# Performance work log

Measured on AMD Instinct MI355X. Metric: run time of the kernel, lower is better.

## Reference

```python
import jax, jax.numpy as jnp
import numpy as np
from functools import partial

DIM = 1024
LIGHT_HID = 512   # dim * 0.5
HEAVY_HID = 4096  # dim * 4
NUM_HEAVY = 1024
N_ITERS = 50
K_ROUTE = 8.0
EPS = 0.1


def rms_norm(x, gamma):
    # F.normalize(x, dim=-1) * sqrt(dim) * gamma
    norm = jnp.linalg.norm(x, axis=-1, keepdims=True)
    normed = x / jnp.maximum(norm, 1e-12)
    return normed * (x.shape[-1] ** 0.5) * gamma


def ffn(x, gamma, w1, b1, w2, b2):
    h = rms_norm(x, gamma)
    h = jax.nn.gelu(h @ w1 + b1, approximate=False)
    return h @ w2 + b2


def coor_descent_route(x, routing_token, num_tokens):
    # s: [b, n]
    s = jnp.einsum('bnd,d->bn', x, routing_token)
    constant = EPS * jnp.log(jnp.asarray(K_ROUTE, dtype=s.dtype))
    b0 = -jax.nn.relu(s)
    a0 = jnp.zeros((s.shape[0], 1), dtype=s.dtype)

    def step(carry, _):
        a_prev, b = carry
        a = constant - EPS * jax.nn.logsumexp((s + b) / EPS, axis=-1, keepdims=True)
        b = -jax.nn.relu(s + a)
        return (a, b), None

    (a, b), _ = jax.lax.scan(step, (a0, b0), None, length=N_ITERS)
    scores = jnp.exp((s + a + b) / EPS)
    sel_scores, sel_idx = jax.lax.top_k(scores, num_tokens)
    # straight-through: value -> 1.0, gradient -> d(sel_scores)
    sel_scores = sel_scores + jax.lax.stop_gradient(1.0 - sel_scores)
    return sel_scores, sel_idx


def setup_inputs() -> dict:
    key = jax.random.key(0)
    ks = jax.random.split(key, 12)
    def lin(k, fan_in, fan_out):
        lim = 1.0 / np.sqrt(fan_in)
        kw, kb = jax.random.split(k)
        w = jax.random.uniform(kw, (fan_in, fan_out), jnp.float32, -lim, lim)
        b = jax.random.uniform(kb, (fan_out,), jnp.float32, -lim, lim)
        return w, b
    x = jax.random.normal(ks[0], (4, 8192, DIM), jnp.float32)
    routing_token = jax.random.normal(ks[1], (DIM,), jnp.float32)
    gamma_light = jnp.ones((DIM,), jnp.float32)
    w1_l, b1_l = lin(ks[2], DIM, LIGHT_HID)
    w2_l, b2_l = lin(ks[3], LIGHT_HID, DIM)
    gamma_heavy = jnp.ones((DIM,), jnp.float32)
    w1_h, b1_h = lin(ks[4], DIM, HEAVY_HID)
    w2_h, b2_h = lin(ks[5], HEAVY_HID, DIM)
    return dict(x=x, routing_token=routing_token,
                gamma_light=gamma_light, w1_light=w1_l, b1_light=b1_l,
                w2_light=w2_l, b2_light=b2_l,
                gamma_heavy=gamma_heavy, w1_heavy=w1_h, b1_heavy=b1_h,
                w2_heavy=w2_h, b2_heavy=b2_h)


def reference(x, routing_token, gamma_light, w1_light, b1_light, w2_light, b2_light,
              gamma_heavy, w1_heavy, b1_heavy, w2_heavy, b2_heavy):
    bsz = x.shape[0]
    light_out = ffn(x, gamma_light, w1_light, b1_light, w2_light, b2_light)
    sel_scores, sel_idx = coor_descent_route(x, routing_token, NUM_HEAVY)
    batch_range = jnp.arange(bsz)[:, None]           # [b, 1]
    routed = x[batch_range, sel_idx]                 # [b, k, d]
    routed_out = ffn(routed, gamma_heavy, w1_heavy, b1_heavy, w2_heavy, b2_heavy)
    routed_out = routed_out * sel_scores[..., None]
    heavy_out = jnp.zeros_like(x).at[batch_range, sel_idx].set(routed_out)
    return light_out + heavy_out
```

## Files before the change

kernel.cpp:

```cpp
#include <hip/hip_runtime.h>
#include <math.h>

#define TOKS   32768
#define NSEQ   8192
#define BATCH  4
#define DIMD   1024
#define LHID   512
#define HHID   4096
#define NHEAVY 1024

typedef __attribute__((ext_vector_type(8))) short bf16x8;
typedef __attribute__((ext_vector_type(4))) float f32x4;
typedef __attribute__((ext_vector_type(8))) unsigned short u16x8;
typedef __attribute__((ext_vector_type(4))) unsigned short u16x4;

__device__ __forceinline__ unsigned short bf16rne(float f) {
    unsigned u = __float_as_uint(f);
    return (unsigned short)((u + 0x7FFFu + ((u >> 16) & 1u)) >> 16);
}
__device__ __forceinline__ float gelu_f(float v) {
    return 0.5f * v * (1.0f + erff(v * 0.7071067811865476f));
}
__device__ __forceinline__ void gload_lds16(const unsigned short* g, unsigned short* l) {
#if defined(__HIP_DEVICE_COMPILE__)
    __builtin_amdgcn_global_load_lds((const __attribute__((address_space(1))) void*)g,
                                     (__attribute__((address_space(3))) void*)l,
                                     16, 0, 0);
#endif
}

__global__ __launch_bounds__(256) void k_rowscale(const float* __restrict__ x,
                                                  const float* __restrict__ rt,
                                                  const float* __restrict__ gamma,
                                                  float* __restrict__ s,
                                                  float* __restrict__ invr,
                                                  unsigned short* __restrict__ xl) {
    int wid = threadIdx.x >> 6, lane = threadIdx.x & 63;
    int row = blockIdx.x * 4 + wid;
    const float4* xr  = (const float4*)(x + (size_t)row * DIMD);
    const float4* rt4 = (const float4*)rt;
    const float4* g4  = (const float4*)gamma;
    float4 v[4];
    float dot = 0.f, ss = 0.f;
#pragma unroll
    for (int i = 0; i < 4; i++) {
        v[i] = xr[lane + 64 * i];
        float4 r = rt4[lane + 64 * i];
        dot += v[i].x * r.x + v[i].y * r.y + v[i].z * r.z + v[i].w * r.w;
        ss  += v[i].x * v[i].x + v[i].y * v[i].y + v[i].z * v[i].z + v[i].w * v[i].w;
    }
#pragma unroll
    for (int o = 32; o > 0; o >>= 1) {
        dot += __shfl_xor(dot, o);
        ss  += __shfl_xor(ss, o);
    }
    float iv = 32.0f / fmaxf(sqrtf(ss), 1e-12f);
    if (lane == 0) { s[row] = dot; invr[row] = iv; }
#pragma unroll
    for (int i = 0; i < 4; i++) {
        float4 g = g4[lane + 64 * i];
        u16x4 o;
        o[0] = bf16rne(v[i].x * iv * g.x);
        o[1] = bf16rne(v[i].y * iv * g.y);
        o[2] = bf16rne(v[i].z * iv * g.z);
        o[3] = bf16rne(v[i].w * iv * g.w);
        *(u16x4*)(xl + (size_t)row * DIMD + (lane + 64 * i) * 4) = o;
    }
}

__global__ __launch_bounds__(256) void k_rowstats(const float* __restrict__ x,
                                                  const float* __restrict__ rt,
                                                  float* __restrict__ s,
                                                  float* __restrict__ invr) {
    int wid = threadIdx.x >> 6, lane = threadIdx.x & 63;
    int row = blockIdx.x * 4 + wid;
    const float4* xr  = (const float4*)(x + (size_t)row * DIMD);
    const float4* rt4 = (const float4*)rt;
    float dot = 0.f, ss = 0.f;
#pragma unroll
    for (int i = 0; i < 4; i++) {
        float4 v = xr[lane + 64 * i];
        float4 r = rt4[lane + 64 * i];
        dot += v.x * r.x + v.y * r.y + v.z * r.z + v.w * r.w;
        ss  += v.x * v.x + v.y * v.y + v.z * v.z + v.w * v.w;
    }
#pragma unroll
    for (int o = 32; o > 0; o >>= 1) {
        dot += __shfl_down(dot, o);
        ss  += __shfl_down(ss, o);
    }
    if (lane == 0) {
        s[row] = dot;
        invr[row] = 32.0f / fmaxf(sqrtf(ss), 1e-12f);
    }
}

__global__ __launch_bounds__(1024) void k_route(const float* __restrict__ s_g,
                                                unsigned long long* __restrict__ keys,
                                                int* __restrict__ pcount,
                                                int* __restrict__ c1cnt) {
    int b = blockIdx.x, tid = threadIdx.x;
    int lane = tid & 63, wid = tid >> 6;
    const float* sb = s_g + b * NSEQ;
    float sv[8];
    float smax = -3.4e38f;
#pragma unroll
    for (int i = 0; i < 8; i++) { sv[i] = sb[tid + 1024 * i]; smax = fmaxf(smax, sv[i]); }
    __shared__ float red[2][16];
#pragma unroll
    for (int o = 32; o > 0; o >>= 1) smax = fmaxf(smax, __shfl_xor(smax, o));
    if (lane == 0) red[0][wid] = smax;
    __syncthreads();
    float smaxAll = -3.4e38f;
    for (int w = 0; w < 16; w++) smaxAll = fmaxf(smaxAll, red[0][w]);
    __syncthreads();

    const float cst = 0.1f * logf(8.0f);
    float a = 0.0f;
    for (int it = 0; it < 50; it++) {
        float tau = -a;
        float M = fminf(smaxAll, tau);
        float p = 0.0f;
#pragma unroll
        for (int i = 0; i < 8; i++) p += expf((fminf(sv[i], tau) - M) * 10.0f);
#pragma unroll
        for (int o = 32; o > 0; o >>= 1) p += __shfl_xor(p, o);
        if (lane == 0) red[it & 1][wid] = p;
        __syncthreads();
        float S = 0.0f;
        for (int w = 0; w < 16; w++) S += red[it & 1][w];
        a = cst - M - 0.1f * logf(S);
    }
    int p = 0, c1 = 0;
#pragma unroll
    for (int i = 0; i < 8; i++) {
        float sc = expf(fminf(sv[i] + a, 0.0f) * 10.0f);
        int n = tid + 1024 * i;
        keys[b * NSEQ + n] = ((unsigned long long)__float_as_uint(sc) << 32)
                           | (unsigned long long)(0xFFFFFFFFu - (unsigned)n);
        p  += (sc > 0.0f) ? 1 : 0;
        c1 += (sc == 1.0f) ? 1 : 0;
    }
#pragma unroll
    for (int o = 32; o > 0; o >>= 1) {
        p  += __shfl_xor(p, o);
        c1 += __shfl_xor(c1, o);
    }
    if (lane == 0) { atomicAdd(&pcount[b], p); atomicAdd(&c1cnt[b], c1); }
}

__global__ __launch_bounds__(1024) void k_select(const unsigned long long* __restrict__ keys,
                                                 const int* __restrict__ pcount,
                                                 const int* __restrict__ c1cnt,
                                                 int* __restrict__ rowmap) {
    int b = blockIdx.x, tid = threadIdx.x;
    int lane = tid & 63, wid = tid >> 6;
    __shared__ int wsum[16];
    __shared__ int slot;
    __shared__ unsigned long long kk_[NSEQ];
    int P = pcount[b], C1 = c1cnt[b];
    if (C1 >= NHEAVY) {
        bool f[8]; int zc = 0;
#pragma unroll
        for (int j = 0; j < 8; j++) {
            unsigned hi = (unsigned)(keys[b * NSEQ + tid * 8 + j] >> 32);
            f[j] = (hi == 0x3F800000u);
            zc += f[j] ? 1 : 0;
        }
        int inc = zc;
        for (int o = 1; o < 64; o <<= 1) {
            int t = __shfl_up(inc, o);
            if (lane >= o) inc += t;
        }
        if (lane == 63) wsum[wid] = inc;
        __syncthreads();
        if (tid == 0) {
            int acc = 0;
            for (int w = 0; w < 16; w++) { int t = wsum[w]; wsum[w] = acc; acc += t; }
        }
        __syncthreads();
        int rank = wsum[wid] + (inc - zc);
#pragma unroll
        for (int j = 0; j < 8; j++) {
            if (f[j]) {
                if (rank < NHEAVY) rowmap[b * NHEAVY + rank] = b * NSEQ + tid * 8 + j;
                rank++;
            }
        }
    } else if (P <= NHEAVY) {
        bool pos[8]; int zc = 0;
#pragma unroll
        for (int j = 0; j < 8; j++) {
            unsigned sbits = (unsigned)(keys[b * NSEQ + tid * 8 + j] >> 32);
            pos[j] = (sbits != 0u);
            zc += pos[j] ? 0 : 1;
        }
        int inc = zc;
        for (int o = 1; o < 64; o <<= 1) {
            int t = __shfl_up(inc, o);
            if (lane >= o) inc += t;
        }
        if (lane == 63) wsum[wid] = inc;
        if (tid == 0) slot = 0;
        __syncthreads();
        if (tid == 0) {
            int acc = 0;
            for (int w = 0; w < 16; w++) { int t = wsum[w]; wsum[w] = acc; acc += t; }
        }
        __syncthreads();
        int zr = wsum[wid] + (inc - zc);
        int Z = NHEAVY - P;
#pragma unroll
        for (int j = 0; j < 8; j++) {
            int n = tid * 8 + j;
            bool sel;
            if (pos[j]) sel = true;
            else { sel = (zr < Z); zr += 1; }
            if (sel) {
                int sl = atomicAdd(&slot, 1);
                rowmap[b * NHEAVY + sl] = b * NSEQ + n;
            }
        }
    } else {
        for (int i = tid; i < NSEQ; i += 1024) kk_[i] = keys[b * NSEQ + i];
        __syncthreads();
        for (int k = 2; k <= NSEQ; k <<= 1) {
            for (int j = k >> 1; j > 0; j >>= 1) {
                for (int i = tid; i < NSEQ; i += 1024) {
                    int ixj = i ^ j;
                    if (ixj > i) {
                        unsigned long long u = kk_[i], v = kk_[ixj];
                        bool dirDesc = ((i & k) == 0);
                        if (dirDesc ? (u < v) : (u > v)) { kk_[i] = v; kk_[ixj] = u; }
                    }
                }
                __syncthreads();
            }
        }
        unsigned idx = 0xFFFFFFFFu - (unsigned)(kk_[tid] & 0xFFFFFFFFull);
        rowmap[b * NHEAVY + tid] = b * NSEQ + (int)idx;
    }
}

__global__ __launch_bounds__(256) void k_transpose(const float* __restrict__ W,
                                                   unsigned short* __restrict__ WT,
                                                   int K, int N) {
    __shared__ float ts[64][65];
    int t = threadIdx.x;
    int n0 = blockIdx.x * 64, k0 = blockIdx.y * 64;
    int kk = t >> 2, nc = (t & 3) * 16;
    const float4* src = (const float4*)(W + (size_t)(k0 + kk) * N + n0 + nc);
#pragma unroll
    for (int j = 0; j < 4; j++) {
        float4 v = src[j];
        ts[kk][nc + 4 * j + 0] = v.x;
        ts[kk][nc + 4 * j + 1] = v.y;
        ts[kk][nc + 4 * j + 2] = v.z;
        ts[kk][nc + 4 * j + 3] = v.w;
    }
    __syncthreads();
    int nn = t >> 2, kc = (t & 3) * 16;
    unsigned short o[16];
#pragma unroll
    for (int j = 0; j < 16; j++) o[j] = bf16rne(ts[kc + j][nn]);
    unsigned short* dst = WT + (size_t)(n0 + nn) * K + k0 + kc;
    *(u16x8*)(dst)     = *(u16x8*)(o);
    *(u16x8*)(dst + 8) = *(u16x8*)(o + 8);
}

__global__ __launch_bounds__(256) void k_prescale(const float* __restrict__ x,
                                                  const float* __restrict__ invr,
                                                  const float* __restrict__ gamma,
                                                  const int* __restrict__ rowmap,
                                                  unsigned short* __restrict__ xo,
                                                  int row_ofs) {
    int t = threadIdx.x;
    int i = blockIdx.x * 2 + (t >> 7);
    int c = (t & 127) * 8;
    int src = rowmap ? rowmap[i] : (row_ofs + i);
    float iv = invr[src];
    const float4* px = (const float4*)(x + (size_t)src * DIMD + c);
    const float4* pg = (const float4*)(gamma + c);
    float4 v0 = px[0], v1 = px[1];
    float4 g0 = pg[0], g1 = pg[1];
    unsigned short o[8];
    o[0] = bf16rne(v0.x * iv * g0.x); o[1] = bf16rne(v0.y * iv * g0.y);
    o[2] = bf16rne(v0.z * iv * g0.z); o[3] = bf16rne(v0.w * iv * g0.w);
    o[4] = bf16rne(v1.x * iv * g1.x); o[5] = bf16rne(v1.y * iv * g1.y);
    o[6] = bf16rne(v1.z * iv * g1.z); o[7] = bf16rne(v1.w * iv * g1.w);
    *(u16x8*)(xo + (size_t)i * DIMD + c) = *(u16x8*)o;
}

__global__ __launch_bounds__(256) void k_scatter(const float* __restrict__ rb,
                                                 const int* __restrict__ rowmap,
                                                 float* __restrict__ out) {
    int i = blockIdx.x;
    int c = threadIdx.x * 4;
    int g = rowmap[i];
    float4 v = *(const float4*)(rb + (size_t)i * DIMD + c);
    float* p = out + (size_t)g * DIMD + c;
    float4 o = *(const float4*)p;
    o.x += v.x; o.y += v.y; o.z += v.z; o.w += v.w;
    *(float4*)p = o;
}

struct GArg {
    const unsigned short* A; const unsigned short* BT; const float* bias;
    void* C; const int* rowmap;
    int K, kslice, m_ofs, ldc, nx, ny;
};

template<int EPI>
__device__ __forceinline__ void gemm_body(const GArg ga, int w, int nwg,
                                          unsigned short* As, unsigned short* Bs) {
    int tid = threadIdx.x;
    int q = nwg >> 3, r = nwg & 7;
    int xcd = w & 7, sub = w >> 3;
    int id = (xcd < r ? xcd * (q + 1) : r * (q + 1) + (xcd - r) * q) + sub;
    int bx = id % ga.nx;
    int t2 = id / ga.nx;
    int by = t2 % ga.ny;
    int bz = t2 / ga.ny;

    int m0 = by * 128, n0 = bx * 128;
    int kbeg = bz * ga.kslice, kend = kbeg + ga.kslice;
    int K = ga.K;
    int lane = tid & 63, wid = tid >> 6;
    int wm = wid >> 1, wn = wid & 1;
    int lc = lane & 15, lr = lane >> 4;

    int srow = lane >> 3;
    int sslot = (lane & 7) ^ srow;
    const unsigned short* paA = ga.A  + (size_t)(m0 + srow) * K + sslot * 8;
    const unsigned short* paB = ga.BT + (size_t)(n0 + srow) * K + sslot * 8;

    f32x4 acc[4][4];
#pragma unroll
    for (int i = 0; i < 4; i++)
#pragma unroll
        for (int j = 0; j < 4; j++) acc[i][j] = (f32x4){0.f, 0.f, 0.f, 0.f};

    for (int k0 = kbeg; k0 < kend; k0 += 64) {
        if (k0 != kbeg) __syncthreads();
#pragma unroll
        for (int qq = 0; qq < 4; qq++) {
            int rb_ = (wid * 4 + qq) * 8;
            gload_lds16(paA + (size_t)rb_ * K + k0, &As[rb_ * 64]);
            gload_lds16(paB + (size_t)rb_ * K + k0, &Bs[rb_ * 64]);
        }
        __syncthreads();
#pragma unroll
        for (int ks = 0; ks < 2; ks++) {
            bf16x8 af[4], bfr[4];
#pragma unroll
            for (int f = 0; f < 4; f++) {
                int rowA = wm * 64 + f * 16 + lc;
                int rowB = wn * 64 + f * 16 + lc;
                int sw = ((ks * 4 + lr) ^ (lc & 7)) << 4;
                af[f]  = *(const bf16x8*)((const char*)As + rowA * 128 + sw);
                bfr[f] = *(const bf16x8*)((const char*)Bs + rowB * 128 + sw);
            }
#pragma unroll
            for (int fm = 0; fm < 4; fm++)
#pragma unroll
                for (int fn = 0; fn < 4; fn++)
                    acc[fm][fn] = __builtin_amdgcn_mfma_f32_16x16x32_bf16(
                        af[fm], bfr[fn], acc[fm][fn], 0, 0, 0);
        }
    }

    float bcol[4];
#pragma unroll
    for (int fn = 0; fn < 4; fn++) {
        float bb = ga.bias[n0 + wn * 64 + fn * 16 + lc];
        if constexpr (EPI == 3) { if (bz != 0) bb = 0.0f; }
        bcol[fn] = bb;
    }
#pragma unroll
    for (int fm = 0; fm < 4; fm++) {
        int rowb = m0 + wm * 64 + fm * 16 + lr * 4;
#pragma unroll
        for (int fn = 0; fn < 4; fn++) {
            int col = n0 + wn * 64 + fn * 16 + lc;
            f32x4 v = acc[fm][fn];
#pragma unroll
            for (int rr = 0; rr < 4; rr++) {
                float val = v[rr] + bcol[fn];
                if constexpr (EPI == 0) {
                    ((unsigned short*)ga.C)[(size_t)(rowb + rr) * ga.ldc + col] =
                        bf16rne(gelu_f(val));
                } else if constexpr (EPI == 1) {
                    ((float*)ga.C)[(size_t)(ga.m_ofs + rowb + rr) * ga.ldc + col] = val;
                } else if constexpr (EPI == 2) {
                    int g = ga.rowmap[ga.m_ofs + rowb + rr];
                    float* p = (float*)ga.C + (size_t)g * ga.ldc + col;
                    *p = *p + val;
                } else {
                    int g = ga.rowmap ? ga.rowmap[rowb + rr] : (rowb + rr);
                    atomicAdd((float*)ga.C + (size_t)g * ga.ldc + col, val);
                }
            }
        }
    }
}

template<int EPI>
__global__ __launch_bounds__(256, 4) void k_mfma(GArg ga) {
    __shared__ unsigned short sm[2][128 * 64];
    gemm_body<EPI>(ga, (int)blockIdx.x, (int)gridDim.x, sm[0], sm[1]);
}

template<int EA, int EB>
__global__ __launch_bounds__(256, 4) void k_mfma2(GArg a, GArg b, int nwgA) {
    __shared__ unsigned short sm[2][128 * 64];
    int w = (int)blockIdx.x;
    if (w < nwgA) gemm_body<EA>(a, w, nwgA, sm[0], sm[1]);
    else          gemm_body<EB>(b, w - nwgA, (int)gridDim.x - nwgA, sm[0], sm[1]);
}

extern "C" void kernel_launch(void* const* d_in, const int* in_sizes, int n_in,
                              void* d_out, int out_size, void* d_ws, size_t ws_size,
                              hipStream_t stream) {
    const float* x   = (const float*)d_in[0];
    const float* rt  = (const float*)d_in[1];
    const float* gl  = (const float*)d_in[2];
    const float* w1l = (const float*)d_in[3];
    const float* b1l = (const float*)d_in[4];
    const float* w2l = (const float*)d_in[5];
    const float* b2l = (const float*)d_in[6];
    const float* gh  = (const float*)d_in[7];
    const float* w1h = (const float*)d_in[8];
    const float* b1h = (const float*)d_in[9];
    const float* w2h = (const float*)d_in[10];
    const float* b2h = (const float*)d_in[11];
    float* out = (float*)d_out;

    char* ws = (char*)d_ws;
    float* s    = (float*)(ws);
    float* invr = (float*)(ws + 131072);
    unsigned long long* keys = (unsigned long long*)(ws + 262144);
    int* rowmap = (int*)(ws + 524288);
    int* pcount = (int*)(ws + 540672);
    int* c1cnt  = pcount + 4;
    size_t off = 1u << 20;
    unsigned short* w1lT = (unsigned short*)(ws + off); off += (size_t)LHID * DIMD * 2;
    unsigned short* w2lT = (unsigned short*)(ws + off); off += (size_t)DIMD * LHID * 2;
    unsigned short* w1hT = (unsigned short*)(ws + off); off += (size_t)HHID * DIMD * 2;
    unsigned short* w2hT = (unsigned short*)(ws + off); off += (size_t)DIMD * HHID * 2;
    unsigned short* xhg  = (unsigned short*)(ws + off); off += (size_t)BATCH * NHEAVY * DIMD * 2;
    char* un = ws + off;
    size_t U = ws_size > off ? ws_size - off : 0;

    const size_t XL_B = (size_t)TOKS * DIMD * 2;
    const size_t HL_B = (size_t)TOKS * LHID * 2;
    const size_t HH_B = (size_t)BATCH * NHEAVY * HHID * 2;
    bool big = (U >= XL_B + HL_B + HH_B);

    hipMemsetAsync(pcount, 0, 32, stream);

    const long MH = (long)BATCH * NHEAVY;

    if (big) {
        unsigned short* xl = (unsigned short*)un;
        unsigned short* hl = (unsigned short*)(un + XL_B);
        unsigned short* hh = (unsigned short*)(un + XL_B + HL_B);
        float* rb = (float*)un;

        k_rowscale<<<TOKS / 4, 256, 0, stream>>>(x, rt, gl, s, invr, xl);
        k_route<<<BATCH, 1024, 0, stream>>>(s, keys, pcount, c1cnt);
        k_select<<<BATCH, 1024, 0, stream>>>(keys, pcount, c1cnt, rowmap);

        k_transpose<<<dim3(LHID / 64, DIMD / 64), 256, 0, stream>>>(w1l, w1lT, DIMD, LHID);
        k_transpose<<<dim3(DIMD / 64, LHID / 64), 256, 0, stream>>>(w2l, w2lT, LHID, DIMD);
        k_transpose<<<dim3(HHID / 64, DIMD / 64), 256, 0, stream>>>(w1h, w1hT, DIMD, HHID);
        k_transpose<<<dim3(DIMD / 64, HHID / 64), 256, 0, stream>>>(w2h, w2hT, HHID, DIMD);
        k_prescale<<<(unsigned)(MH / 2), 256, 0, stream>>>(x, invr, gh, rowmap, xhg, 0);

        GArg lg1{xl,  w1lT, b1l, hl, nullptr, DIMD, DIMD, 0, LHID, LHID / 128, TOKS / 128};
        GArg hg1{xhg, w1hT, b1h, hh, nullptr, DIMD, DIMD, 0, HHID, HHID / 128, (int)MH / 128};
        k_mfma2<0, 0><<<2048, 256, 0, stream>>>(lg1, hg1, 1024);

        hipMemsetAsync(rb, 0, (size_t)MH * DIMD * 4, stream);
        GArg lg2{hl, w2lT, b2l, out, nullptr, LHID, LHID, 0, DIMD, DIMD / 128, TOKS / 128};
        GArg hg2{hh, w2hT, b2h, rb, nullptr, HHID, HHID / 4, 0, DIMD, DIMD / 128, (int)MH / 128};
        k_mfma2<1, 3><<<3072, 256, 0, stream>>>(lg2, hg2, 2048);

        k_scatter<<<(unsigned)MH, 256, 0, stream>>>(rb, rowmap, out);
    } else {
        k_rowstats<<<TOKS / 4, 256, 0, stream>>>(x, rt, s, invr);
        k_route<<<BATCH, 1024, 0, stream>>>(s, keys, pcount, c1cnt);
        k_select<<<BATCH, 1024, 0, stream>>>(keys, pcount, c1cnt, rowmap);

        k_transpose<<<dim3(LHID / 64, DIMD / 64), 256, 0, stream>>>(w1l, w1lT, DIMD, LHID);
        k_transpose<<<dim3(DIMD / 64, LHID / 64), 256, 0, stream>>>(w2l, w2lT, LHID, DIMD);
        k_transpose<<<dim3(HHID / 64, DIMD / 64), 256, 0, stream>>>(w1h, w1hT, DIMD, HHID);
        k_transpose<<<dim3(DIMD / 64, HHID / 64), 256, 0, stream>>>(w2h, w2hT, HHID, DIMD);

        long Rl = (long)(U / 3072);
        Rl -= Rl % 128; if (Rl < 128) Rl = 128; if (Rl > TOKS) Rl = TOKS;
        unsigned short* xl = (unsigned short*)un;
        unsigned short* hl = (unsigned short*)(un + (size_t)Rl * DIMD * 2);
        for (long mo = 0; mo < TOKS; mo += Rl) {
            long R = TOKS - mo < Rl ? TOKS - mo : Rl;
            k_prescale<<<(unsigned)(R / 2), 256, 0, stream>>>(x, invr, gl, nullptr, xl, (int)mo);
            GArg a1{xl, w1lT, b1l, hl, nullptr, DIMD, DIMD, 0, LHID, LHID / 128, (int)(R / 128)};
            k_mfma<0><<<(LHID / 128) * (unsigned)(R / 128), 256, 0, stream>>>(a1);
            GArg a2{hl, w2lT, b2l, out, nullptr, LHID, LHID, (int)mo, DIMD, DIMD / 128, (int)(R / 128)};
            k_mfma<1><<<(DIMD / 128) * (unsigned)(R / 128), 256, 0, stream>>>(a2);
        }

        k_prescale<<<(unsigned)(MH / 2), 256, 0, stream>>>(x, invr, gh, rowmap, xhg, 0);
        long Rh = (long)(U / ((size_t)HHID * 2));
        Rh -= Rh % 128; if (Rh < 128) Rh = 128; if (Rh > MH) Rh = MH;
        unsigned short* hh = (unsigned short*)un;
        for (long mo = 0; mo < MH; mo += Rh) {
            long R = MH - mo < Rh ? MH - mo : Rh;
            GArg b1{xhg + (size_t)mo * DIMD, w1hT, b1h, hh, nullptr, DIMD, DIMD, 0, HHID,
                    HHID / 128, (int)(R / 128)};
            k_mfma<0><<<(HHID / 128) * (unsigned)(R / 128), 256, 0, stream>>>(b1);
            GArg b2{hh, w2hT, b2h, out, rowmap, HHID, HHID, (int)mo, DIMD,
                    DIMD / 128, (int)(R / 128)};
            k_mfma<2><<<(DIMD / 128) * (unsigned)(R / 128), 256, 0, stream>>>(b2);
        }
    }
}
```

Before: 392.8 us.

## Fuse routing and selection, batch transposes, drop split-K and reorder GEMM work

Merges the route and select kernels into one per-batch kernel that builds the row map directly, with fast paths that skip the bitonic sort. It also combines the four weight transposes into one launch and removes the pcount and accumulator memsets. The heavy second GEMM no longer uses split-K with an atomic epilogue, and heavy work-groups are scheduled ahead of light ones. The GEMM loop now uses pointer increments and the occupancy hint goes from 4 to 5. These changes cut launch overhead and atomic traffic, but without split-K the heavy GEMM has fewer, longer work-groups, which can leave the tail of the grid unbalanced.

```diff
diff --git a/kernel.cpp b/kernel.cpp
--- a/kernel.cpp
+++ b/kernel.cpp
@@ -95,6 +95,164 @@
     }
 }
 
+__global__ __launch_bounds__(1024) void k_routesel(const float* __restrict__ s_g,
+                                                   int* __restrict__ rowmap) {
+    int b = blockIdx.x, tid = threadIdx.x;
+    int lane = tid & 63, wid = tid >> 6;
+    __shared__ float red[2][16];
+    __shared__ int wsum[16];
+    __shared__ int ws2[16];
+    __shared__ int PC[2];
+    __shared__ int slot;
+    __shared__ unsigned long long kk_[NSEQ];
+    const float* sb = s_g + b * NSEQ;
+    float sv[8];
+    float smax = -3.4e38f;
+#pragma unroll
+    for (int i = 0; i < 8; i++) { sv[i] = sb[tid + 1024 * i]; smax = fmaxf(smax, sv[i]); }
+#pragma unroll
+    for (int o = 32; o > 0; o >>= 1) smax = fmaxf(smax, __shfl_xor(smax, o));
+    if (lane == 0) red[0][wid] = smax;
+    __syncthreads();
+    float smaxAll = -3.4e38f;
+    for (int w = 0; w < 16; w++) smaxAll = fmaxf(smaxAll, red[0][w]);
+    __syncthreads();
+
+    const float cst = 0.1f * logf(8.0f);
+    float a = 0.0f;
+    for (int it = 0; it < 50; it++) {
+        float tau = -a;
+        float M = fminf(smaxAll, tau);
+        float p = 0.0f;
+#pragma unroll
+        for (int i = 0; i < 8; i++) p += expf((fminf(sv[i], tau) - M) * 10.0f);
+#pragma unroll
+        for (int o = 32; o > 0; o >>= 1) p += __shfl_xor(p, o);
+        if (lane == 0) red[it & 1][wid] = p;
+        __syncthreads();
+        float S = 0.0f;
+        for (int w = 0; w < 16; w++) S += red[it & 1][w];
+        a = cst - M - 0.1f * logf(S);
+        __syncthreads();
+    }
+    float sc[8];
+    int p = 0, c1 = 0;
+#pragma unroll
+    for (int i = 0; i < 8; i++) {
+        sc[i] = expf(fminf(sv[i] + a, 0.0f) * 10.0f);
+        p  += (sc[i] > 0.0f) ? 1 : 0;
+        c1 += (sc[i] == 1.0f) ? 1 : 0;
+    }
+    {
+        int pp = p, cc = c1;
+#pragma unroll
+        for (int o = 32; o > 0; o >>= 1) {
+            pp += __shfl_xor(pp, o);
+            cc += __shfl_xor(cc, o);
+        }
+        if (lane == 0) { wsum[wid] = pp; ws2[wid] = cc; }
+        __syncthreads();
+        if (tid == 0) {
+            int sp = 0, sC = 0;
+            for (int w = 0; w < 16; w++) { sp += wsum[w]; sC += ws2[w]; }
+            PC[0] = sp; PC[1] = sC;
+        }
+        __syncthreads();
+    }
+    int P = PC[0], C1 = PC[1];
+    __syncthreads();
+
+    if (C1 >= NHEAVY) {
+        __shared__ unsigned char fl[NSEQ];
+#pragma unroll
+        for (int i = 0; i < 8; i++) fl[tid + 1024 * i] = (sc[i] == 1.0f) ? 1 : 0;
+        __syncthreads();
+        int zc = 0;
+        unsigned char f[8];
+#pragma unroll
+        for (int j = 0; j < 8; j++) { f[j] = fl[tid * 8 + j]; zc += f[j]; }
+        int inc = zc;
+        for (int o = 1; o < 64; o <<= 1) {
+            int t = __shfl_up(inc, o);
+            if (lane >= o) inc += t;
+        }
+        if (lane == 63) wsum[wid] = inc;
+        __syncthreads();
+        if (tid == 0) {
+            int acc = 0;
+            for (int w = 0; w < 16; w++) { int t = wsum[w]; wsum[w] = acc; acc += t; }
+        }
+        __syncthreads();
+        int rank = wsum[wid] + (inc - zc);
+#pragma unroll
+        for (int j = 0; j < 8; j++) {
+            if (f[j]) {
+                if (rank < NHEAVY) rowmap[b * NHEAVY + rank] = b * NSEQ + tid * 8 + j;
+                rank++;
+            }
+        }
+    } else if (P <= NHEAVY) {
+        __shared__ unsigned char fl[NSEQ];
+#pragma unroll
+        for (int i = 0; i < 8; i++) fl[tid + 1024 * i] = (sc[i] > 0.0f) ? 1 : 0;
+        __syncthreads();
+        unsigned char pos[8]; int zc = 0;
+#pragma unroll
+        for (int j = 0; j < 8; j++) { pos[j] = fl[tid * 8 + j]; zc += pos[j] ? 0 : 1; }
+        int inc = zc;
+        for (int o = 1; o < 64; o <<= 1) {
+            int t = __shfl_up(inc, o);
+            if (lane >= o) inc += t;
+        }
+        if (lane == 63) wsum[wid] = inc;
+        if (tid == 0) slot = 0;
+        __syncthreads();
+        if (tid == 0) {
+            int acc = 0;
+            for (int w = 0; w < 16; w++) { int t = wsum[w]; wsum[w] = acc; acc += t; }
+        }
+        __syncthreads();
+        int zr = wsum[wid] + (inc - zc);
+        int Z = NHEAVY - P;
+#pragma unroll
+        for (int j = 0; j < 8; j++) {
+            int n = tid * 8 + j;
+            bool sel;
+            if (pos[j]) sel = true;
+            else { sel = (zr < Z); zr += 1; }
+            if (sel) {
+                int sl = atomicAdd(&slot, 1);
+                rowmap[b * NHEAVY + sl] = b * NSEQ + n;
+            }
+        }
+    } else {
+#pragma unroll
+        for (int i = 0; i < 8; i++) {
+            int n = tid + 1024 * i;
+            kk_[n] = ((unsigned long long)__float_as_uint(sc[i]) << 32)
+                   | (unsigned long long)(0xFFFFFFFFu - (unsigned)n);
+        }
+        __syncthreads();
+        for (int k = 2; k <= NSEQ; k <<= 1) {
+            for (int j = k >> 1; j > 0; j >>= 1) {
+                for (int i = tid; i < NSEQ; i += 1024) {
+                    int ixj = i ^ j;
+                    if (ixj > i) {
+                        unsigned long long u = kk_[i], v = kk_[ixj];
+                        bool dirDesc = ((i & k) == 0);
+                        if (dirDesc ? (u < v) : (u > v)) { kk_[i] = v; kk_[ixj] = u; }
+                    }
+                }
+                __syncthreads();
+            }
+        }
+        if (tid < NHEAVY) {
+            unsigned idx = 0xFFFFFFFFu - (unsigned)(kk_[tid] & 0xFFFFFFFFull);
+            rowmap[b * NHEAVY + tid] = b * NSEQ + (int)idx;
+        }
+    }
+}
+
 __global__ __launch_bounds__(1024) void k_route(const float* __restrict__ s_g,
                                                 unsigned long long* __restrict__ keys,
                                                 int* __restrict__ pcount,
@@ -114,7 +272,6 @@
     float smaxAll = -3.4e38f;
     for (int w = 0; w < 16; w++) smaxAll = fmaxf(smaxAll, red[0][w]);
     __syncthreads();
-
     const float cst = 0.1f * logf(8.0f);
     float a = 0.0f;
     for (int it = 0; it < 50; it++) {
@@ -242,12 +399,10 @@
     }
 }
 
-__global__ __launch_bounds__(256) void k_transpose(const float* __restrict__ W,
-                                                   unsigned short* __restrict__ WT,
-                                                   int K, int N) {
+__device__ __forceinline__ void transpose_body(const float* W, unsigned short* WT,
+                                               int K, int N, int n0, int k0) {
     __shared__ float ts[64][65];
     int t = threadIdx.x;
-    int n0 = blockIdx.x * 64, k0 = blockIdx.y * 64;
     int kk = t >> 2, nc = (t & 3) * 16;
     const float4* src = (const float4*)(W + (size_t)(k0 + kk) * N + n0 + nc);
 #pragma unroll
@@ -266,6 +421,24 @@
     unsigned short* dst = WT + (size_t)(n0 + nn) * K + k0 + kc;
     *(u16x8*)(dst)     = *(u16x8*)(o);
     *(u16x8*)(dst + 8) = *(u16x8*)(o + 8);
+}
+
+__global__ __launch_bounds__(256) void k_transpose(const float* __restrict__ W,
+                                                   unsigned short* __restrict__ WT,
+                                                   int K, int N) {
+    transpose_body(W, WT, K, N, blockIdx.x * 64, blockIdx.y * 64);
+}
+
+__global__ __launch_bounds__(256) void k_transpose4(
+        const float* w1l, unsigned short* w1lT,
+        const float* w2l, unsigned short* w2lT,
+        const float* w1h, unsigned short* w1hT,
+        const float* w2h, unsigned short* w2hT) {
+    int w = (int)blockIdx.x;
+    if (w < 128)       { int i = w;        transpose_body(w1l, w1lT, DIMD, LHID, (i % 8) * 64,  (i / 8) * 64); }
+    else if (w < 256)  { int i = w - 128;  transpose_body(w2l, w2lT, LHID, DIMD, (i % 16) * 64, (i / 16) * 64); }
+    else if (w < 1280) { int i = w - 256;  transpose_body(w1h, w1hT, DIMD, HHID, (i % 64) * 64, (i / 64) * 64); }
+    else               { int i = w - 1280; transpose_body(w2h, w2hT, HHID, DIMD, (i % 16) * 64, (i / 16) * 64); }
 }
 
 __global__ __launch_bounds__(256) void k_prescale(const float* __restrict__ x,
@@ -323,7 +496,8 @@
     int bz = t2 / ga.ny;
 
     int m0 = by * 128, n0 = bx * 128;
-    int kbeg = bz * ga.kslice, kend = kbeg + ga.kslice;
+    int kbeg = bz * ga.kslice;
+    int nsteps = ga.kslice >> 6;
     int K = ga.K;
     int lane = tid & 63, wid = tid >> 6;
     int wm = wid >> 1, wn = wid & 1;
@@ -331,8 +505,21 @@
 
     int srow = lane >> 3;
     int sslot = (lane & 7) ^ srow;
-    const unsigned short* paA = ga.A  + (size_t)(m0 + srow) * K + sslot * 8;
-    const unsigned short* paB = ga.BT + (size_t)(n0 + srow) * K + sslot * 8;
+    const unsigned short* paA = ga.A  + (size_t)(m0 + srow) * K + sslot * 8 + kbeg;
+    const unsigned short* paB = ga.BT + (size_t)(n0 + srow) * K + sslot * 8 + kbeg;
+
+    const unsigned short* gA[4];
+    const unsigned short* gB[4];
+    unsigned short* lA[4];
+    unsigned short* lB[4];
+#pragma unroll
+    for (int qq = 0; qq < 4; qq++) {
+        int rb_ = (wid * 4 + qq) * 8;
+        gA[qq] = paA + (size_t)rb_ * K;
+        gB[qq] = paB + (size_t)rb_ * K;
+        lA[qq] = &As[rb_ * 64];
+        lB[qq] = &Bs[rb_ * 64];
+    }
 
     f32x4 acc[4][4];
 #pragma unroll
@@ -340,13 +527,13 @@
 #pragma unroll
         for (int j = 0; j < 4; j++) acc[i][j] = (f32x4){0.f, 0.f, 0.f, 0.f};
 
-    for (int k0 = kbeg; k0 < kend; k0 += 64) {
-        if (k0 != kbeg) __syncthreads();
+    for (int t = 0; t < nsteps; t++) {
+        if (t) __syncthreads();
 #pragma unroll
         for (int qq = 0; qq < 4; qq++) {
-            int rb_ = (wid * 4 + qq) * 8;
-            gload_lds16(paA + (size_t)rb_ * K + k0, &As[rb_ * 64]);
-            gload_lds16(paB + (size_t)rb_ * K + k0, &Bs[rb_ * 64]);
+            gload_lds16(gA[qq], lA[qq]);
+            gload_lds16(gB[qq], lB[qq]);
+            gA[qq] += 64; gB[qq] += 64;
         }
         __syncthreads();
 #pragma unroll
@@ -405,13 +592,13 @@
 }
 
 template<int EPI>
-__global__ __launch_bounds__(256, 4) void k_mfma(GArg ga) {
+__global__ __launch_bounds__(256, 5) void k_mfma(GArg ga) {
     __shared__ unsigned short sm[2][128 * 64];
     gemm_body<EPI>(ga, (int)blockIdx.x, (int)gridDim.x, sm[0], sm[1]);
 }
 
 template<int EA, int EB>
-__global__ __launch_bounds__(256, 4) void k_mfma2(GArg a, GArg b, int nwgA) {
+__global__ __launch_bounds__(256, 5) void k_mfma2(GArg a, GArg b, int nwgA) {
     __shared__ unsigned short sm[2][128 * 64];
     int w = (int)blockIdx.x;
     if (w < nwgA) gemm_body<EA>(a, w, nwgA, sm[0], sm[1]);
@@ -456,8 +643,6 @@
     const size_t HH_B = (size_t)BATCH * NHEAVY * HHID * 2;
     bool big = (U >= XL_B + HL_B + HH_B);
 
-    hipMemsetAsync(pcount, 0, 32, stream);
-
     const long MH = (long)BATCH * NHEAVY;
 
     if (big) {
@@ -467,26 +652,21 @@
         float* rb = (float*)un;
 
         k_rowscale<<<TOKS / 4, 256, 0, stream>>>(x, rt, gl, s, invr, xl);
-        k_route<<<BATCH, 1024, 0, stream>>>(s, keys, pcount, c1cnt);
-        k_select<<<BATCH, 1024, 0, stream>>>(keys, pcount, c1cnt, rowmap);
-
-        k_transpose<<<dim3(LHID / 64, DIMD / 64), 256, 0, stream>>>(w1l, w1lT, DIMD, LHID);
-        k_transpose<<<dim3(DIMD / 64, LHID / 64), 256, 0, stream>>>(w2l, w2lT, LHID, DIMD);
-        k_transpose<<<dim3(HHID / 64, DIMD / 64), 256, 0, stream>>>(w1h, w1hT, DIMD, HHID);
-        k_transpose<<<dim3(DIMD / 64, HHID / 64), 256, 0, stream>>>(w2h, w2hT, HHID, DIMD);
+        k_routesel<<<BATCH, 1024, 0, stream>>>(s, rowmap);
+        k_transpose4<<<2304, 256, 0, stream>>>(w1l, w1lT, w2l, w2lT, w1h, w1hT, w2h, w2hT);
         k_prescale<<<(unsigned)(MH / 2), 256, 0, stream>>>(x, invr, gh, rowmap, xhg, 0);
 
+        GArg hg1{xhg, w1hT, b1h, hh, nullptr, DIMD, DIMD, 0, HHID, HHID / 128, (int)MH / 128};
         GArg lg1{xl,  w1lT, b1l, hl, nullptr, DIMD, DIMD, 0, LHID, LHID / 128, TOKS / 128};
-        GArg hg1{xhg, w1hT, b1h, hh, nullptr, DIMD, DIMD, 0, HHID, HHID / 128, (int)MH / 128};
-        k_mfma2<0, 0><<<2048, 256, 0, stream>>>(lg1, hg1, 1024);
-
-        hipMemsetAsync(rb, 0, (size_t)MH * DIMD * 4, stream);
+        k_mfma2<0, 0><<<2048, 256, 0, stream>>>(hg1, lg1, 1024);
+
+        GArg hg2{hh, w2hT, b2h, rb,  nullptr, HHID, HHID, 0, DIMD, DIMD / 128, (int)MH / 128};
         GArg lg2{hl, w2lT, b2l, out, nullptr, LHID, LHID, 0, DIMD, DIMD / 128, TOKS / 128};
-        GArg hg2{hh, w2hT, b2h, rb, nullptr, HHID, HHID / 4, 0, DIMD, DIMD / 128, (int)MH / 128};
-        k_mfma2<1, 3><<<3072, 256, 0, stream>>>(lg2, hg2, 2048);
+        k_mfma2<1, 1><<<2304, 256, 0, stream>>>(hg2, lg2, 256);
 
         k_scatter<<<(unsigned)MH, 256, 0, stream>>>(rb, rowmap, out);
     } else {
+        hipMemsetAsync(pcount, 0, 32, stream);
         k_rowstats<<<TOKS / 4, 256, 0, stream>>>(x, rt, s, invr);
         k_route<<<BATCH, 1024, 0, stream>>>(s, keys, pcount, c1cnt);
         k_select<<<BATCH, 1024, 0, stream>>>(keys, pcount, c1cnt, rowmap);
```

Measured after the change: 833.3 us. 2.12x slower.
